# Kernel optimization log

Measured on AMD Instinct MI355X. Metric: run time of the kernel, lower is better.

The kernel has to match this reference:

```python
import math
import jax, jax.numpy as jnp
import numpy as np

MAX_SEQ = 4096
NEG_INF = float("-inf")

def _causal_mask(max_seq):
    # 0 on/below diagonal, -inf above (standard additive causal mask)
    i = jnp.arange(max_seq)[:, None]
    j = jnp.arange(max_seq)[None, :]
    return jnp.where(j <= i, 0.0, NEG_INF).astype(jnp.float32)

def setup_inputs() -> dict:
    key = jax.random.key(0)
    ks = jax.random.split(key, 5)
    bsz, seqlen, n_heads, n_kv_heads, head_dim = 1, 2048, 32, 8, 128
    return {
        "input_pos": jnp.arange(seqlen, dtype=jnp.int64 if jax.config.jax_enable_x64 else jnp.int32),
        "q": jax.random.normal(ks[0], (bsz, seqlen, n_heads, head_dim), dtype=jnp.float32),
        "k": jax.random.normal(ks[1], (bsz, seqlen, n_kv_heads, head_dim), dtype=jnp.float32),
        "v": jax.random.normal(ks[2], (bsz, seqlen, n_kv_heads, head_dim), dtype=jnp.float32),
        "bsz": bsz,
        "seqlen": seqlen,
        "mask": _causal_mask(MAX_SEQ),
        "k_cache": jax.random.normal(ks[3], (bsz, n_kv_heads, MAX_SEQ, head_dim), dtype=jnp.float32),
        "v_cache": jax.random.normal(ks[4], (bsz, n_kv_heads, MAX_SEQ, head_dim), dtype=jnp.float32),
    }

def reference(input_pos, q, k, v, bsz, seqlen, mask, k_cache, v_cache):
    # [b, s, h, d] -> [b, h, s, d]
    qt = jnp.swapaxes(q, 1, 2)
    kt = jnp.swapaxes(k, 1, 2)
    vt = jnp.swapaxes(v, 1, 2)
    # KV-cache update at input_pos along the seq axis
    kc = k_cache.at[:, :, input_pos].set(kt)   # [b, hkv, T, d], T = MAX_SEQ
    vc = v_cache.at[:, :, input_pos].set(vt)
    n_rep = qt.shape[1] // kc.shape[1]
    # GQA head expansion (repeat_interleave along head axis)
    kr = jnp.repeat(kc, n_rep, axis=1)          # [b, h, T, d]
    vr = jnp.repeat(vc, n_rep, axis=1)
    attn_mask = mask[input_pos][None, None]     # [1, 1, s, T]
    scale = 1.0 / math.sqrt(qt.shape[-1])
    w = jnp.einsum("bhsd,bhtd->bhst", qt, kr) * scale + attn_mask
    w = jax.nn.softmax(w, axis=-1)
    y = jnp.einsum("bhst,bhtd->bhsd", w, vr)    # [b, h, s, d]
    return jnp.swapaxes(y, 1, 2).reshape(bsz, seqlen, -1)
```

## Files before the change

kernel.cpp:

```cpp
#include <hip/hip_runtime.h>
#include <hip/hip_bf16.h>

typedef __bf16 bf16_t;
typedef bf16_t bf16x8 __attribute__((ext_vector_type(8)));
typedef float f32x16 __attribute__((ext_vector_type(16)));

#define NH    32
#define NKV   8
#define HD    128
#define OUTD  4096
#define SEQ   2048
#define KVBLK 64
#define KB_SZ 16384
#define VB_SZ 16384
#define KP_BYTES (NKV * SEQ * HD * 2)

__device__ __forceinline__ float fexp2(float x) {
    return __builtin_amdgcn_exp2f(x);
}

__device__ __forceinline__ unsigned cvtpk(float lo, float hi) {
    unsigned r;
    asm("v_cvt_pk_bf16_f32 %0, %1, %2" : "=v"(r) : "v"(lo), "v"(hi));
    return r;
}

__device__ __forceinline__ uint4 pack8u(float4 a, float4 b) {
    union { bf16_t h[8]; uint4 u; } t;
    t.h[0] = (bf16_t)a.x; t.h[1] = (bf16_t)a.y; t.h[2] = (bf16_t)a.z; t.h[3] = (bf16_t)a.w;
    t.h[4] = (bf16_t)b.x; t.h[5] = (bf16_t)b.y; t.h[6] = (bf16_t)b.z; t.h[7] = (bf16_t)b.w;
    return t.u;
}

extern "C" __global__ __launch_bounds__(256)
void prep_k_kernel(const float* __restrict__ k, bf16_t* __restrict__ kp) {
    const size_t idx = ((size_t)blockIdx.x * 256 + threadIdx.x) * 8;
    const int d   = idx & 127;
    const int s   = (int)((idx >> 7) & 2047);
    const int hkv = (int)(idx >> 18);
    const float* src = k + (((size_t)s * NKV + hkv) << 7) + d;
    float4 a = *(const float4*)src;
    float4 b = *(const float4*)(src + 4);
    *(uint4*)(kp + idx) = pack8u(a, b);
}

extern "C" __global__ __launch_bounds__(256)
void prep_v_kernel(const float* __restrict__ v, bf16_t* __restrict__ vp) {
    __shared__ bf16_t tile[64][132];
    const int hkv = blockIdx.x >> 5;
    const int tau = blockIdx.x & 31;
    const int kvr = threadIdx.x >> 2;
    const int c0  = (threadIdx.x & 3) << 5;
    const float* src = v + (((size_t)((tau << 6) + kvr) * NKV + hkv) << 7) + c0;
    #pragma unroll
    for (int i = 0; i < 8; ++i) {
        float4 a = ((const float4*)src)[i];
        tile[kvr][c0 + 4 * i + 0] = (bf16_t)a.x;
        tile[kvr][c0 + 4 * i + 1] = (bf16_t)a.y;
        tile[kvr][c0 + 4 * i + 2] = (bf16_t)a.z;
        tile[kvr][c0 + 4 * i + 3] = (bf16_t)a.w;
    }
    __syncthreads();
    const int d  = threadIdx.x >> 1;
    const int kh = (threadIdx.x & 1) << 5;
    union { bf16_t h[32]; uint4 u[4]; } o;
    #pragma unroll
    for (int i = 0; i < 32; ++i) o.h[i] = tile[kh + i][d];
    bf16_t* dst = vp + ((((size_t)hkv * 32 + tau) * 128 + d) << 6) + kh;
    #pragma unroll
    for (int i = 0; i < 4; ++i) ((uint4*)dst)[i] = o.u[i];
}

extern "C" __global__ __launch_bounds__(512, 2)
void sdpa_fwd_kernel(const float* __restrict__ qsrc,
                     const bf16_t* __restrict__ kp,
                     const bf16_t* __restrict__ vp,
                     float* __restrict__ out)
{
    __shared__ __align__(16) unsigned char k_lds[2 * KB_SZ];
    __shared__ __align__(16) unsigned char v_lds[2 * VB_SZ];

    const int tid  = threadIdx.x;
    const int l    = tid & 63;
    const int wave = tid >> 6;
    const int l31  = l & 31;
    const int hb   = l >> 5;
    const int x7   = l & 7;

    const int bid  = blockIdx.x;
    const int hkv  = bid & 7;
    const int head = (hkv << 2) + ((bid >> 3) & 3);
    const int p    = bid >> 5;
    const int qt   = (wave < 4) ? p : (15 - p);
    const int qb   = (qt << 7) + ((wave & 3) << 5);
    const int qrow = qb + l31;

    bf16x8 qf[8];
    {
        const float sc = 0.08838834764831845f * 1.4426950408889634f;
        const float* qp = qsrc + ((size_t)qrow * NH + head) * HD + (hb << 3);
        #pragma unroll
        for (int kk = 0; kk < 8; ++kk) {
            float4 a = *(const float4*)(qp + kk * 16);
            float4 b = *(const float4*)(qp + kk * 16 + 4);
            bf16x8 f;
            f[0] = (bf16_t)(a.x * sc); f[1] = (bf16_t)(a.y * sc);
            f[2] = (bf16_t)(a.z * sc); f[3] = (bf16_t)(a.w * sc);
            f[4] = (bf16_t)(b.x * sc); f[5] = (bf16_t)(b.y * sc);
            f[6] = (bf16_t)(b.z * sc); f[7] = (bf16_t)(b.w * sc);
            qf[kk] = f;
        }
    }

    float m_run = -__builtin_inff();
    float l_run = 0.f;
    f32x16 yacc[4];
    #pragma unroll
    for (int db = 0; db < 4; ++db) yacc[db] = (f32x16)0.f;

    const int nt_b = 32 - 2 * p;
    const int ntw  = (qb >> 6) + 1;

    const bf16_t* kbase = kp + (size_t)hkv * (SEQ * HD);
    const bf16_t* vbase = vp + (size_t)hkv * (32 * HD * 64);

    uint4 kst0, kst1, vst0, vst1;
    auto issue = [&](int t) {
        const unsigned char* kt = (const unsigned char*)(kbase + (size_t)(t << 6) * HD);
        const unsigned char* vt = (const unsigned char*)(vbase + (size_t)t * (HD * 64));
        kst0 = *(const uint4*)(kt + tid * 16);
        kst1 = *(const uint4*)(kt + (tid + 512) * 16);
        vst0 = *(const uint4*)(vt + tid * 16);
        vst1 = *(const uint4*)(vt + (tid + 512) * 16);
    };
    auto writeL = [&](int buf) {
        unsigned char* kb = k_lds + buf * KB_SZ;
        unsigned char* vb = v_lds + buf * VB_SZ;
        {
            int s = tid;
            *(uint4*)(kb + ((s >> 4) << 8) + (((s & 15) ^ ((s >> 4) & 7)) << 4)) = kst0;
            s = tid + 512;
            *(uint4*)(kb + ((s >> 4) << 8) + (((s & 15) ^ ((s >> 4) & 7)) << 4)) = kst1;
        }
        {
            int s = tid;
            *(uint4*)(vb + ((s >> 3) << 7) + (((s & 7) ^ ((s >> 3) & 7)) << 4)) = vst0;
            s = tid + 512;
            *(uint4*)(vb + ((s >> 3) << 7) + (((s & 7) ^ ((s >> 3) & 7)) << 4)) = vst1;
        }
    };

    issue(0);
    writeL(0);
    __syncthreads();

    for (int t = 0; t < nt_b; ++t) {
        const bool pre = (t + 1 < nt_b);
        if (pre) issue(t + 1);

        if (t < ntw) {
            const unsigned char* kb  = k_lds + (t & 1) * KB_SZ;
            const unsigned char* vtb = v_lds + (t & 1) * VB_SZ;
            const int  kv0     = t << 6;
            const bool last    = (t == ntw - 1);
            const int  thalves = (!last || (qb & 32)) ? 2 : 1;

            f32x16 st[2];
            #pragma unroll
            for (int tt = 0; tt < 2; ++tt) st[tt] = (f32x16)0.f;
            __builtin_amdgcn_s_setprio(1);
            #pragma unroll
            for (int tt = 0; tt < 2; ++tt) {
                if (tt >= thalves) continue;
                #pragma unroll
                for (int kk = 0; kk < 8; ++kk) {
                    const bf16x8 kf = *(const bf16x8*)(kb + (tt << 13) + (l31 << 8)
                                                       + (((((kk << 1) | hb)) ^ x7) << 4));
                    st[tt] = __builtin_amdgcn_mfma_f32_32x32x16_bf16(kf, qf[kk], st[tt], 0, 0, 0);
                }
            }
            __builtin_amdgcn_s_setprio(0);

            if (last) {
                #pragma unroll
                for (int tt = 0; tt < 2; ++tt) {
                    if (tt >= thalves) continue;
                    if (kv0 + (tt << 5) + 31 > qb) {
                        #pragma unroll
                        for (int r = 0; r < 16; ++r) {
                            const int kv = kv0 + (tt << 5) + (r & 3) + ((r >> 2) << 3) + (hb << 2);
                            if (kv > qrow) st[tt][r] = -__builtin_inff();
                        }
                    }
                }
            }

            float pmax = -__builtin_inff();
            #pragma unroll
            for (int tt = 0; tt < 2; ++tt) {
                if (tt >= thalves) continue;
                #pragma unroll
                for (int r = 0; r < 16; ++r) pmax = fmaxf(pmax, st[tt][r]);
            }
            pmax = fmaxf(pmax, __shfl_xor(pmax, 32));

            float corr = 1.0f;
            if (!__all(pmax <= m_run + 8.0f)) {
                const float mnew = fmaxf(m_run, pmax);
                corr = fexp2(m_run - mnew);
                m_run = mnew;
                #pragma unroll
                for (int db = 0; db < 4; ++db) yacc[db] *= corr;
            }

            float ssum = 0.f;
            #pragma unroll
            for (int tt = 0; tt < 2; ++tt) {
                if (tt >= thalves) continue;
                #pragma unroll
                for (int r = 0; r < 16; ++r) {
                    const float pe = fexp2(st[tt][r] - m_run);
                    st[tt][r] = pe;
                    ssum += pe;
                }
            }
            ssum += __shfl_xor(ssum, 32);
            l_run = l_run * corr + ssum;

            bf16x8 pa[4];
            #pragma unroll
            for (int tt = 0; tt < 2; ++tt) {
                if (tt >= thalves) continue;
                #pragma unroll
                for (int sp = 0; sp < 2; ++sp) {
                    const unsigned wA0 = cvtpk(st[tt][8 * sp + 0], st[tt][8 * sp + 1]);
                    const unsigned wA1 = cvtpk(st[tt][8 * sp + 2], st[tt][8 * sp + 3]);
                    const unsigned wB0 = cvtpk(st[tt][8 * sp + 4], st[tt][8 * sp + 5]);
                    const unsigned wB1 = cvtpk(st[tt][8 * sp + 6], st[tt][8 * sp + 7]);
                    const unsigned sA0 = (unsigned)__shfl_xor((int)wA0, 32);
                    const unsigned sA1 = (unsigned)__shfl_xor((int)wA1, 32);
                    const unsigned sB0 = (unsigned)__shfl_xor((int)wB0, 32);
                    const unsigned sB1 = (unsigned)__shfl_xor((int)wB1, 32);
                    uint4 w;
                    w.x = hb ? sB0 : wA0;
                    w.y = hb ? sB1 : wA1;
                    w.z = hb ? wB0 : sA0;
                    w.w = hb ? wB1 : sA1;
                    pa[2 * tt + sp] = __builtin_bit_cast(bf16x8, w);
                }
            }

            const int kslim = thalves << 1;
            __builtin_amdgcn_s_setprio(1);
            #pragma unroll
            for (int db = 0; db < 4; ++db) {
                #pragma unroll
                for (int ks = 0; ks < 4; ++ks) {
                    if (ks >= kslim) continue;
                    const bf16x8 vf = *(const bf16x8*)(vtb + ((l31 + (db << 5)) << 7)
                                                       + (((((ks << 1) | hb)) ^ x7) << 4));
                    yacc[db] = __builtin_amdgcn_mfma_f32_32x32x16_bf16(vf, pa[ks], yacc[db], 0, 0, 0);
                }
            }
            __builtin_amdgcn_s_setprio(0);
        }

        if (pre) {
            writeL((t + 1) & 1);
            __syncthreads();
        }
    }

    const float inv = 1.0f / l_run;
    float* op = out + (size_t)qrow * OUTD + head * HD;
    #pragma unroll
    for (int db = 0; db < 4; ++db) {
        #pragma unroll
        for (int r = 0; r < 16; ++r) {
            const int d = (db << 5) + (r & 3) + ((r >> 2) << 3) + (hb << 2);
            op[d] = yacc[db][r] * inv;
        }
    }
}

extern "C" void kernel_launch(void* const* d_in, const int* in_sizes, int n_in,
                              void* d_out, int out_size, void* d_ws, size_t ws_size,
                              hipStream_t stream) {
    const float* q = (const float*)d_in[1];
    const float* k = (const float*)d_in[2];
    const float* v = (const float*)d_in[3];
    float* out = (float*)d_out;

    bf16_t* kp = (bf16_t*)d_ws;
    bf16_t* vp = (bf16_t*)((char*)d_ws + KP_BYTES);

    prep_k_kernel<<<dim3(NKV * SEQ * HD / (256 * 8)), dim3(256), 0, stream>>>(k, kp);
    prep_v_kernel<<<dim3(NKV * (SEQ / KVBLK)), dim3(256), 0, stream>>>(v, vp);
    sdpa_fwd_kernel<<<dim3(256), dim3(512), 0, stream>>>(q, kp, vp, out);
}
```

Baseline: 228.0 us.

## Split attention blocks into 4-wave single-tile blocks with single-buffered LDS

Drops the paired causal-balancing of two query tiles per 512-thread block. Each 256-thread block now handles one 128-row query tile, launched heaviest-first across 512 blocks. K/V staging drops from double-buffered to single-buffered LDS, with an extra barrier before each overwrite, and launch bounds change to allow 4 blocks per CU. The aim is better occupancy and dynamic load balancing, at the cost of losing compute/LDS-write overlap and adding synchronisation.

```diff
diff --git a/kernel.cpp b/kernel.cpp
--- a/kernel.cpp
+++ b/kernel.cpp
@@ -71,14 +71,14 @@
     for (int i = 0; i < 4; ++i) ((uint4*)dst)[i] = o.u[i];
 }
 
-extern "C" __global__ __launch_bounds__(512, 2)
+extern "C" __global__ __launch_bounds__(256, 4)
 void sdpa_fwd_kernel(const float* __restrict__ qsrc,
                      const bf16_t* __restrict__ kp,
                      const bf16_t* __restrict__ vp,
                      float* __restrict__ out)
 {
-    __shared__ __align__(16) unsigned char k_lds[2 * KB_SZ];
-    __shared__ __align__(16) unsigned char v_lds[2 * VB_SZ];
+    __shared__ __align__(16) unsigned char k_lds[KB_SZ];
+    __shared__ __align__(16) unsigned char v_lds[VB_SZ];
 
     const int tid  = threadIdx.x;
     const int l    = tid & 63;
@@ -89,10 +89,11 @@
 
     const int bid  = blockIdx.x;
     const int hkv  = bid & 7;
-    const int head = (hkv << 2) + ((bid >> 3) & 3);
-    const int p    = bid >> 5;
-    const int qt   = (wave < 4) ? p : (15 - p);
-    const int qb   = (qt << 7) + ((wave & 3) << 5);
+    const int rest = bid >> 3;
+    const int head = (hkv << 2) + (rest & 3);
+    const int qt   = 15 - (rest >> 2);
+
+    const int qb   = (qt << 7) + (wave << 5);
     const int qrow = qb + l31;
 
     bf16x8 qf[8];
@@ -118,40 +119,33 @@
     #pragma unroll
     for (int db = 0; db < 4; ++db) yacc[db] = (f32x16)0.f;
 
-    const int nt_b = 32 - 2 * p;
+    const int nt_b = 2 * qt + 2;
     const int ntw  = (qb >> 6) + 1;
 
     const bf16_t* kbase = kp + (size_t)hkv * (SEQ * HD);
     const bf16_t* vbase = vp + (size_t)hkv * (32 * HD * 64);
 
-    uint4 kst0, kst1, vst0, vst1;
+    uint4 kst[4], vst[4];
     auto issue = [&](int t) {
         const unsigned char* kt = (const unsigned char*)(kbase + (size_t)(t << 6) * HD);
         const unsigned char* vt = (const unsigned char*)(vbase + (size_t)t * (HD * 64));
-        kst0 = *(const uint4*)(kt + tid * 16);
-        kst1 = *(const uint4*)(kt + (tid + 512) * 16);
-        vst0 = *(const uint4*)(vt + tid * 16);
-        vst1 = *(const uint4*)(vt + (tid + 512) * 16);
+        #pragma unroll
+        for (int i = 0; i < 4; ++i) {
+            kst[i] = *(const uint4*)(kt + (tid + 256 * i) * 16);
+            vst[i] = *(const uint4*)(vt + (tid + 256 * i) * 16);
+        }
     };
-    auto writeL = [&](int buf) {
-        unsigned char* kb = k_lds + buf * KB_SZ;
-        unsigned char* vb = v_lds + buf * VB_SZ;
-        {
-            int s = tid;
-            *(uint4*)(kb + ((s >> 4) << 8) + (((s & 15) ^ ((s >> 4) & 7)) << 4)) = kst0;
-            s = tid + 512;
-            *(uint4*)(kb + ((s >> 4) << 8) + (((s & 15) ^ ((s >> 4) & 7)) << 4)) = kst1;
-        }
-        {
-            int s = tid;
-            *(uint4*)(vb + ((s >> 3) << 7) + (((s & 7) ^ ((s >> 3) & 7)) << 4)) = vst0;
-            s = tid + 512;
-            *(uint4*)(vb + ((s >> 3) << 7) + (((s & 7) ^ ((s >> 3) & 7)) << 4)) = vst1;
+    auto writeL = [&]() {
+        #pragma unroll
+        for (int i = 0; i < 4; ++i) {
+            const int s = tid + 256 * i;
+            *(uint4*)(k_lds + ((s >> 4) << 8) + (((s & 15) ^ ((s >> 4) & 7)) << 4)) = kst[i];
+            *(uint4*)(v_lds + ((s >> 3) << 7) + (((s & 7) ^ ((s >> 3) & 7)) << 4)) = vst[i];
         }
     };
 
     issue(0);
-    writeL(0);
+    writeL();
     __syncthreads();
 
     for (int t = 0; t < nt_b; ++t) {
@@ -159,8 +153,6 @@
         if (pre) issue(t + 1);
 
         if (t < ntw) {
-            const unsigned char* kb  = k_lds + (t & 1) * KB_SZ;
-            const unsigned char* vtb = v_lds + (t & 1) * VB_SZ;
             const int  kv0     = t << 6;
             const bool last    = (t == ntw - 1);
             const int  thalves = (!last || (qb & 32)) ? 2 : 1;
@@ -174,7 +166,7 @@
                 if (tt >= thalves) continue;
                 #pragma unroll
                 for (int kk = 0; kk < 8; ++kk) {
-                    const bf16x8 kf = *(const bf16x8*)(kb + (tt << 13) + (l31 << 8)
+                    const bf16x8 kf = *(const bf16x8*)(k_lds + (tt << 13) + (l31 << 8)
                                                        + (((((kk << 1) | hb)) ^ x7) << 4));
                     st[tt] = __builtin_amdgcn_mfma_f32_32x32x16_bf16(kf, qf[kk], st[tt], 0, 0, 0);
                 }
@@ -257,7 +249,7 @@
                 #pragma unroll
                 for (int ks = 0; ks < 4; ++ks) {
                     if (ks >= kslim) continue;
-                    const bf16x8 vf = *(const bf16x8*)(vtb + ((l31 + (db << 5)) << 7)
+                    const bf16x8 vf = *(const bf16x8*)(v_lds + ((l31 + (db << 5)) << 7)
                                                        + (((((ks << 1) | hb)) ^ x7) << 4));
                     yacc[db] = __builtin_amdgcn_mfma_f32_32x32x16_bf16(vf, pa[ks], yacc[db], 0, 0, 0);
                 }
@@ -265,8 +257,9 @@
             __builtin_amdgcn_s_setprio(0);
         }
 
+        __syncthreads();
         if (pre) {
-            writeL((t + 1) & 1);
+            writeL();
             __syncthreads();
         }
     }
@@ -296,5 +289,5 @@
 
     prep_k_kernel<<<dim3(NKV * SEQ * HD / (256 * 8)), dim3(256), 0, stream>>>(k, kp);
     prep_v_kernel<<<dim3(NKV * (SEQ / KVBLK)), dim3(256), 0, stream>>>(v, vp);
-    sdpa_fwd_kernel<<<dim3(256), dim3(512), 0, stream>>>(q, kp, vp, out);
-}
+    sdpa_fwd_kernel<<<dim3(512), dim3(256), 0, stream>>>(q, kp, vp, out);
+}
```

After: 517.1 us. +126.8%, slower.
